# Kernel tuning notes

Measured on AMD Instinct MI355X. Metric: run time of the kernel, lower is better.

## Reference

```python
import jax, jax.numpy as jnp
import numpy as np
import math

B, T, D, H = 16, 256, 1024, 1024
SEG = 16              # segment_len
S = T // SEG          # number of cached segment slots (max_cached_segments=None)
SCALE = 1.0 / math.sqrt(H)


def _ln(x, g, b, eps=1e-5):
    m = jnp.mean(x, -1, keepdims=True)
    v = jnp.mean((x - m) ** 2, -1, keepdims=True)
    return (x - m) * jax.lax.rsqrt(v + eps) * g + b


def _lstm_cell(inp, h, c, Wih, Whh, bih, bhh):
    z = inp @ Wih.T + bih + h @ Whh.T + bhh
    i, f, g, o = jnp.split(z, 4, axis=-1)  # torch LSTMCell gate order i,f,g,o
    c2 = jax.nn.sigmoid(f) * c + jax.nn.sigmoid(i) * jnp.tanh(g)
    return jax.nn.sigmoid(o) * jnp.tanh(c2), c2


def setup_inputs() -> dict:
    key = jax.random.key(0)
    it = iter(jax.random.split(key, 40))

    def un(shape, fan):
        lim = 1.0 / np.sqrt(fan)
        return jax.random.uniform(next(it), shape, jnp.float32, -lim, lim)

    inp = {}
    inp['x'] = jax.random.normal(next(it), (B, T, D), jnp.float32)
    inp['W_ip'] = un((D, D), D); inp['b_ip'] = un((D,), D)
    inp['g_ip'] = jnp.ones((D,), jnp.float32); inp['be_ip'] = jnp.zeros((D,), jnp.float32)
    inp['W_ih0'] = un((4 * H, D), H); inp['W_hh0'] = un((4 * H, H), H)
    inp['b_ih0'] = un((4 * H,), H); inp['b_hh0'] = un((4 * H,), H)
    inp['W_ih1'] = un((4 * H, H), H); inp['W_hh1'] = un((4 * H, H), H)
    inp['b_ih1'] = un((4 * H,), H); inp['b_hh1'] = un((4 * H,), H)
    inp['Wq'] = un((H, H), H); inp['Wk'] = un((H, H), H); inp['Wv'] = un((H, H), H)
    inp['Wg1'] = un((H, 3 * H), 3 * H); inp['bg1'] = un((H,), 3 * H)
    inp['Wg2'] = un((H, H), H); inp['bg2'] = un((H,), H)
    inp['Wo'] = un((H, H), H); inp['bo'] = un((H,), H)
    inp['Wf'] = un((H, 2 * H), 2 * H); inp['bf'] = un((H,), 2 * H)
    inp['g_f'] = jnp.ones((H,), jnp.float32); inp['be_f'] = jnp.zeros((H,), jnp.float32)
    return inp


def reference(x, W_ip, b_ip, g_ip, be_ip,
              W_ih0, W_hh0, b_ih0, b_hh0,
              W_ih1, W_hh1, b_ih1, b_hh1,
              Wq, Wk, Wv, Wg1, bg1, Wg2, bg2, Wo, bo,
              Wf, bf, g_f, be_f):
    # input_proj (eval mode: dropout = identity)
    xp = jax.nn.relu(_ln(x @ W_ip.T + b_ip, g_ip, be_ip))      # [B,T,D]
    xseg = xp.transpose(1, 0, 2).reshape(S, SEG, B, D)          # [S,SEG,B,D]

    def seg_body(carry, xs):
        h0, c0, h1, c1, kbank, vbank = carry
        x_s, s = xs                                             # x_s:[SEG,B,D], s = #cached segments
        valid = jnp.arange(S) < s

        def step(inner, xt):
            h0, c0, h1, c1, seg_sum = inner
            h0, c0 = _lstm_cell(xt, h0, c0, W_ih0, W_hh0, b_ih0, b_hh0)
            h1, c1 = _lstm_cell(h0, h1, c1, W_ih1, W_hh1, b_ih1, b_hh1)
            # SegmentMemoryRetriever, cache_mode='gated_residual'
            q = h1 @ Wq.T
            scores = jnp.einsum('bh,sbh->bs', q, kbank) * SCALE
            scores = jnp.where(valid[None, :], scores, -1e9)
            attn = jax.nn.softmax(scores, axis=-1)
            retrieved = jnp.einsum('bs,sbh->bh', attn, vbank)
            gi = jnp.concatenate([h1, retrieved, h1 - retrieved], -1)
            gate = jax.nn.sigmoid(jax.nn.relu(gi @ Wg1.T + bg1) @ Wg2.T + bg2)
            out = (gate * h1 + (1.0 - gate) * retrieved) @ Wo.T + bo
            ret = jnp.where(s > 0, out, jnp.zeros_like(out))    # empty cache -> zero retrieval
            enh = jax.nn.relu(_ln(jnp.concatenate([h1, ret], -1) @ Wf.T + bf, g_f, be_f))
            return (h0, c0, h1, c1, seg_sum + h1), enh

        init = (h0, c0, h1, c1, jnp.zeros_like(h1))
        (h0, c0, h1, c1, seg_sum), enh = jax.lax.scan(step, init, x_s)
        # append segment to cache; keys/values projected once (linear, equivalent)
        kbank = kbank.at[s].set((seg_sum / SEG) @ Wk.T)         # context = segment mean (use_segment_context)
        vbank = vbank.at[s].set(h1 @ Wv.T)                      # memory = last top hidden of segment
        return (h0, c0, h1, c1, kbank, vbank), enh

    z = jnp.zeros((B, H), x.dtype)
    bank = jnp.zeros((S, B, H), x.dtype)
    carry0 = (z, z, z, z, bank, bank)
    _, enh = jax.lax.scan(seg_body, carry0, (xseg, jnp.arange(S)))
    return enh.reshape(T, B, H).transpose(1, 0, 2)              # sequence_output [B,T,H]
```

## Files before the change

### kernel.cpp

```cpp
#include <hip/hip_runtime.h>
#include <hip/hip_bf16.h>
#include <math.h>

#define B_ 16
#define T_ 256
#define D_ 1024
#define H_ 1024
#define S_ 16
#define SCALE_ (1.0f/32.0f)

typedef __attribute__((ext_vector_type(8))) short short8v;
typedef __attribute__((ext_vector_type(4))) float f32x4;

__device__ __forceinline__ float sigm(float x) { return 1.f / (1.f + expf(-x)); }

__device__ __forceinline__ ushort f2b(float v) {
  __hip_bfloat16 h = __float2bfloat16(v);
  return *reinterpret_cast<ushort*>(&h);
}
__device__ __forceinline__ float b2f(ushort u) {
  union { unsigned u32; float f; } x; x.u32 = ((unsigned)u) << 16; return x.f;
}

__device__ __forceinline__ void glds16(const void* g, void* l) {
  __builtin_amdgcn_global_load_lds((const __attribute__((address_space(1))) void*)g,
                                   (__attribute__((address_space(3))) void*)l, 16, 0, 0);
}

__device__ __forceinline__ void waitflags64(const int* f, int lane) {
  for (;;) {
    int v = __hip_atomic_load(f + lane, __ATOMIC_RELAXED, __HIP_MEMORY_SCOPE_AGENT);
    if (__all(v != 0)) return;
    __builtin_amdgcn_s_sleep(1);
  }
}

__device__ __forceinline__ void publish_pair(ushort* base, int tid, ushort hb) {
  unsigned hi = (unsigned)__shfl_down((int)hb, 1);
  if (!(tid & 1)) {
    unsigned word = (unsigned)hb | (hi << 16);
    __hip_atomic_exchange((unsigned*)base, word,
                          __ATOMIC_RELAXED, __HIP_MEMORY_SCOPE_AGENT);
  }
}

__device__ __forceinline__ float block_sum256(float v) {
  __shared__ float lds[4];
  #pragma unroll
  for (int off = 32; off; off >>= 1) v += __shfl_down(v, off);
  int w = threadIdx.x >> 6;
  if ((threadIdx.x & 63) == 0) lds[w] = v;
  __syncthreads();
  float r = lds[0] + lds[1] + lds[2] + lds[3];
  __syncthreads();
  return r;
}

__global__ __launch_bounds__(256)
void cvt_bf16(const float* __restrict__ in, ushort* __restrict__ out, int n)
{
  int i = (blockIdx.x * 256 + threadIdx.x) * 4;
  if (i >= n) return;
  float4 v = *(const float4*)(in + i);
  ushort4 o; o.x = f2b(v.x); o.y = f2b(v.y); o.z = f2b(v.z); o.w = f2b(v.w);
  *(ushort4*)(out + i) = o;
}

template<int ACT, int REMAP>
__global__ __launch_bounds__(256)
void gemm_bf16(const ushort* __restrict__ A, const ushort* __restrict__ W,
               const float* __restrict__ bias,
               float* __restrict__ Cf, ushort* __restrict__ Cb,
               int M, int N, int K, float ascale)
{
  __shared__ char As[16384];
  __shared__ char Bs[16384];
  const int tid = threadIdx.x;
  const int w = tid >> 6, l = tid & 63;
  const int m0 = blockIdx.y * 128, n0 = blockIdx.x * 128;
  const int wm = w >> 1, wn = w & 1;
  const int srow = l >> 3;
  const int sbyte = ((l & 7) * 16) ^ (srow << 4);
  f32x4 acc[4][4];
  #pragma unroll
  for (int i = 0; i < 4; ++i)
    #pragma unroll
    for (int j = 0; j < 4; ++j) acc[i][j] = (f32x4){0.f, 0.f, 0.f, 0.f};

  for (int k0 = 0; k0 < K; k0 += 64) {
    __syncthreads();
    #pragma unroll
    for (int c = 0; c < 4; ++c) {
      int ca = w * 4 + c;
      int r = ca * 8 + srow;
      glds16((const char*)A + (((size_t)(m0 + r) * K + k0) << 1) + sbyte, As + ca * 1024);
      glds16((const char*)W + (((size_t)(n0 + r) * K + k0) << 1) + sbyte, Bs + ca * 1024);
    }
    __syncthreads();
    #pragma unroll
    for (int ks = 0; ks < 2; ++ks) {
      short8v a[4], b[4];
      int qb = ks * 64 + (l >> 4) * 16;
      #pragma unroll
      for (int i = 0; i < 4; ++i) {
        int ra = wm * 64 + i * 16 + (l & 15);
        a[i] = *(const short8v*)(As + ra * 128 + (qb ^ ((ra & 7) << 4)));
        int rb = wn * 64 + i * 16 + (l & 15);
        b[i] = *(const short8v*)(Bs + rb * 128 + (qb ^ ((rb & 7) << 4)));
      }
      #pragma unroll
      for (int i = 0; i < 4; ++i)
        #pragma unroll
        for (int j = 0; j < 4; ++j)
          acc[i][j] = __builtin_amdgcn_mfma_f32_16x16x32_bf16(a[i], b[j], acc[i][j], 0, 0, 0);
    }
  }
  #pragma unroll
  for (int i = 0; i < 4; ++i) {
    #pragma unroll
    for (int j = 0; j < 4; ++j) {
      int n = n0 + wn * 64 + j * 16 + (l & 15);
      float bv = bias ? bias[n] : 0.f;
      #pragma unroll
      for (int q = 0; q < 4; ++q) {
        int m = m0 + wm * 64 + i * 16 + (l >> 4) * 4 + q;
        float v = acc[i][j][q] * ascale + bv;
        if (ACT == 1) v = fmaxf(v, 0.f);
        if (ACT == 2) v = sigm(v);
        size_t off = REMAP ? ((size_t)((m & 255) * 16 + (m >> 8)) * N + n)
                           : ((size_t)m * N + n);
        if (Cf) Cf[off] = v;
        if (Cb) Cb[off] = f2b(v);
      }
    }
  }
}

__global__ __launch_bounds__(256)
void ln_relu_bf16(const float* __restrict__ X, const float* __restrict__ g,
                  const float* __restrict__ be, ushort* __restrict__ out)
{
  size_t row = blockIdx.x;
  const float4* p = (const float4*)(X + row * 1024);
  int tid = threadIdx.x;
  float4 v = p[tid];
  float s = block_sum256(v.x + v.y + v.z + v.w);
  float mean = s * (1.f / 1024.f);
  float dx = v.x - mean, dy = v.y - mean, dz = v.z - mean, dw = v.w - mean;
  float ss = block_sum256(dx*dx + dy*dy + dz*dz + dw*dw);
  float r = rsqrtf(ss * (1.f / 1024.f) + 1e-5f);
  int c4 = tid * 4;
  ushort4 o;
  o.x = f2b(fmaxf(dx * r * g[c4+0] + be[c4+0], 0.f));
  o.y = f2b(fmaxf(dy * r * g[c4+1] + be[c4+1], 0.f));
  o.z = f2b(fmaxf(dz * r * g[c4+2] + be[c4+2], 0.f));
  o.w = f2b(fmaxf(dw * r * g[c4+3] + be[c4+3], 0.f));
  *(ushort4*)(out + row * 1024 + c4) = o;
}

__global__ __launch_bounds__(256)
void ln_relu_final(const float* __restrict__ F, const float* __restrict__ g,
                   const float* __restrict__ be, float* __restrict__ out)
{
  int row = blockIdx.x;
  int t = row >> 4, b = row & 15;
  const float4* p = (const float4*)(F + (size_t)row * 1024);
  int tid = threadIdx.x;
  float4 v = p[tid];
  float s = block_sum256(v.x + v.y + v.z + v.w);
  float mean = s * (1.f / 1024.f);
  float dx = v.x - mean, dy = v.y - mean, dz = v.z - mean, dw = v.w - mean;
  float ss = block_sum256(dx*dx + dy*dy + dz*dz + dw*dw);
  float r = rsqrtf(ss * (1.f / 1024.f) + 1e-5f);
  int c4 = tid * 4;
  float4 o;
  o.x = fmaxf(dx * r * g[c4+0] + be[c4+0], 0.f);
  o.y = fmaxf(dy * r * g[c4+1] + be[c4+1], 0.f);
  o.z = fmaxf(dz * r * g[c4+2] + be[c4+2], 0.f);
  o.w = fmaxf(dw * r * g[c4+3] + be[c4+3], 0.f);
  ((float4*)(out + ((size_t)b * T_ + t) * 1024))[tid] = o;
}

__global__ __launch_bounds__(512)
void lstm_persistent(const ushort* __restrict__ Z0T,
                     const ushort* __restrict__ whh0,
                     const float* __restrict__ bhh0,
                     const ushort* __restrict__ wih1,
                     const ushort* __restrict__ whh1,
                     const float* __restrict__ bih1,
                     const float* __restrict__ bhh1,
                     ushort* __restrict__ HP,
                     ushort* __restrict__ H1B,
                     const ushort* __restrict__ ZP,
                     float* __restrict__ KSUM,
                     int* flag0,
                     int* flag1)
{
  __shared__ char Ah[65536];
  __shared__ float zs[8][16][16];
  __builtin_amdgcn_fence(__ATOMIC_ACQUIRE, "agent");
  const int tid = threadIdx.x, w = tid >> 6, l = tid & 63;
  const int lm = l & 15, lq = l >> 4;
  const int g = w & 3, kh = w >> 2;
  const int jb = blockIdx.x & 63;
  const int j0 = jb * 16;
  const int eb = tid >> 4, ej = tid & 15, jf = j0 + ej;
  float creg = 0.f;
  float br[4];

  if (blockIdx.x < 64) {
    short8v wreg[16];
    {
      const int n = g * 1024 + j0 + lm;
      const ushort* wb = whh0 + (size_t)n * 1024 + kh * 512 + lq * 8;
      #pragma unroll
      for (int ks = 0; ks < 16; ++ks) wreg[ks] = *(const short8v*)(wb + ks * 32);
    }
    if (tid < 256) {
      #pragma unroll
      for (int gg = 0; gg < 4; ++gg) br[gg] = bhh0[gg * 1024 + jf];
    }
    for (int t = 0; t < T_; ++t) {
      float z0v[4];
      if (tid < 256) {
        const ushort* zp = Z0T + ((size_t)t * 16 + eb) * 4096 + jf;
        #pragma unroll
        for (int gg = 0; gg < 4; ++gg) z0v[gg] = b2f(zp[gg * 1024]);
      }
      if (t > 0) {
        if (w == 0) waitflags64(flag0 + (size_t)t * 64, l);
        __syncthreads();
      }
      const ushort* hin = HP + (size_t)t * 16384;
      #pragma unroll
      for (int it = 0; it < 4; ++it) {
        int g1k = w * 4 + it;
        int kc = g1k * 4 + lq;
        int m = lm ^ (kc & 15);
        glds16(hin + (size_t)m * 1024 + kc * 8, Ah + g1k * 1024);
      }
      __syncthreads();
      {
        f32x4 a0 = {0.f,0.f,0.f,0.f}, a1 = {0.f,0.f,0.f,0.f};
        #pragma unroll
        for (int ks = 0; ks < 16; ks += 2) {
          int kc0 = kh * 64 + ks * 4 + lq;
          int kc1 = kc0 + 4;
          short8v f0 = *(const short8v*)(Ah + kc0 * 256 + ((lm ^ (kc0 & 15)) << 4));
          short8v f1 = *(const short8v*)(Ah + kc1 * 256 + ((lm ^ (kc1 & 15)) << 4));
          a0 = __builtin_amdgcn_mfma_f32_16x16x32_bf16(f0, wreg[ks],     a0, 0, 0, 0);
          a1 = __builtin_amdgcn_mfma_f32_16x16x32_bf16(f1, wreg[ks + 1], a1, 0, 0, 0);
        }
        #pragma unroll
        for (int q = 0; q < 4; ++q) zs[w][lq * 4 + q][lm] = a0[q] + a1[q];
      }
      __syncthreads();
      if (tid < 256) {
        float zi = zs[0][eb][ej] + zs[4][eb][ej] + z0v[0] + br[0];
        float zf = zs[1][eb][ej] + zs[5][eb][ej] + z0v[1] + br[1];
        float zg = zs[2][eb][ej] + zs[6][eb][ej] + z0v[2] + br[2];
        float zo = zs[3][eb][ej] + zs[7][eb][ej] + z0v[3] + br[3];
        float cp = sigm(zf) * creg + sigm(zi) * tanhf(zg);
        creg = cp;
        ushort hb = f2b(sigm(zo) * tanhf(cp));
        publish_pair(HP + (size_t)(t + 1) * 16384 + eb * 1024 + jf, tid, hb);
      }
      __syncthreads();
      if (tid == 0)
        __hip_atomic_store(flag0 + (size_t)(t + 1) * 64 + jb, 1,
                           __ATOMIC_RELAXED, __HIP_MEMORY_SCOPE_AGENT);
    }
  } else {
    short8v wreg[32];
    {
      const int n = g * 1024 + j0 + lm;
      const ushort* wb = (kh ? whh1 : wih1) + (size_t)n * 1024 + lq * 8;
      #pragma unroll
      for (int ks = 0; ks < 32; ++ks) wreg[ks] = *(const short8v*)(wb + ks * 32);
    }
    if (tid < 256) {
      #pragma unroll
      for (int gg = 0; gg < 4; ++gg)
        br[gg] = bih1[gg * 1024 + jf] + bhh1[gg * 1024 + jf];
    }
    float ksr = 0.f;
    for (int t = 0; t < T_; ++t) {
      if (w == 0) waitflags64(flag0 + (size_t)(t + 1) * 64, l);
      __syncthreads();
      const ushort* h0n = HP + (size_t)(t + 1) * 16384;
      #pragma unroll
      for (int it = 0; it < 4; ++it) {
        int g1k = w * 4 + it;
        int kc = g1k * 4 + lq;
        int m = lm ^ (kc & 15);
        glds16(h0n + (size_t)m * 1024 + kc * 8, Ah + g1k * 1024);
      }
      if (w == 1 && t > 0) waitflags64(flag1 + (size_t)(t - 1) * 64, l);
      __syncthreads();
      const ushort* h1p = (t > 0) ? (H1B + (size_t)(t - 1) * 16384) : ZP;
      #pragma unroll
      for (int it = 0; it < 4; ++it) {
        int g1k = 32 + w * 4 + it;
        int kc = g1k * 4 + lq;
        int m = lm ^ (kc & 15);
        glds16(h1p + (size_t)m * 1024 + (kc - 128) * 8, Ah + g1k * 1024);
      }
      __syncthreads();
      {
        f32x4 a0 = {0.f,0.f,0.f,0.f}, a1 = {0.f,0.f,0.f,0.f};
        #pragma unroll
        for (int ks = 0; ks < 32; ks += 2) {
          int kc0 = kh * 128 + ks * 4 + lq;
          int kc1 = kc0 + 4;
          short8v f0 = *(const short8v*)(Ah + kc0 * 256 + ((lm ^ (kc0 & 15)) << 4));
          short8v f1 = *(const short8v*)(Ah + kc1 * 256 + ((lm ^ (kc1 & 15)) << 4));
          a0 = __builtin_amdgcn_mfma_f32_16x16x32_bf16(f0, wreg[ks],     a0, 0, 0, 0);
          a1 = __builtin_amdgcn_mfma_f32_16x16x32_bf16(f1, wreg[ks + 1], a1, 0, 0, 0);
        }
        #pragma unroll
        for (int q = 0; q < 4; ++q) zs[w][lq * 4 + q][lm] = a0[q] + a1[q];
      }
      __syncthreads();
      if (tid < 256) {
        float zi = zs[0][eb][ej] + zs[4][eb][ej] + br[0];
        float zf = zs[1][eb][ej] + zs[5][eb][ej] + br[1];
        float zg = zs[2][eb][ej] + zs[6][eb][ej] + br[2];
        float zo = zs[3][eb][ej] + zs[7][eb][ej] + br[3];
        float cp = sigm(zf) * creg + sigm(zi) * tanhf(zg);
        creg = cp;
        float hv = sigm(zo) * tanhf(cp);
        ksr += hv;
        publish_pair(H1B + (size_t)t * 16384 + eb * 1024 + jf, tid, f2b(hv));
        if ((t & 15) == 15) {
          KSUM[((size_t)(t >> 4) * 16 + eb) * 1024 + jf] = ksr;
          ksr = 0.f;
        }
      }
      __syncthreads();
      if (tid == 0)
        __hip_atomic_store(flag1 + (size_t)t * 64 + jb, 1,
                           __ATOMIC_RELAXED, __HIP_MEMORY_SCOPE_AGENT);
    }
  }
}

__global__ __launch_bounds__(256)
void vgather(const ushort* __restrict__ H1B, ushort* __restrict__ VINB)
{
  int i = blockIdx.x * 256 + threadIdx.x;
  int row = i >> 8, c4 = (i & 255) * 4;
  int src = (row >> 4) * 256 + 240 + (row & 15);
  *(ushort4*)(VINB + (size_t)row * 1024 + c4) =
      *(const ushort4*)(H1B + (size_t)src * 1024 + c4);
}

__global__ __launch_bounds__(256)
void attn_kernel(const float* __restrict__ Q, const float* __restrict__ kbank,
                 const float* __restrict__ vbank, float* __restrict__ R)
{
  int row = blockIdx.x;
  int t = row >> 4, b = row & 15;
  int si = t >> 4;
  int tid = threadIdx.x, lane = tid & 63, w = tid >> 6;
  if (si == 0) {
    float4 z = {0.f, 0.f, 0.f, 0.f};
    ((float4*)(R + (size_t)row * 1024))[tid] = z;
    return;
  }
  __shared__ float sc[16];
  const float* q = Q + (size_t)row * 1024;
  for (int s = w; s < si; s += 4) {
    const float* kk = kbank + ((size_t)s * 16 + b) * 1024;
    float p = 0.f;
    for (int k = lane; k < 1024; k += 64) p += q[k] * kk[k];
    #pragma unroll
    for (int off = 32; off; off >>= 1) p += __shfl_down(p, off);
    if (lane == 0) sc[s] = p * SCALE_;
  }
  __syncthreads();
  float mx = -1e30f;
  for (int s = 0; s < si; ++s) mx = fmaxf(mx, sc[s]);
  float den = 0.f;
  for (int s = 0; s < si; ++s) den += expf(sc[s] - mx);
  float inv = 1.f / den;
  float4 accv = {0.f, 0.f, 0.f, 0.f};
  for (int s = 0; s < si; ++s) {
    float a = expf(sc[s] - mx) * inv;
    float4 vv = ((const float4*)(vbank + ((size_t)s * 16 + b) * 1024))[tid];
    accv.x += a * vv.x; accv.y += a * vv.y; accv.z += a * vv.z; accv.w += a * vv.w;
  }
  ((float4*)(R + (size_t)row * 1024))[tid] = accv;
}

__global__ __launch_bounds__(256)
void build_gi(const ushort* __restrict__ H1B, const float* __restrict__ R,
              ushort* __restrict__ GI)
{
  size_t r = blockIdx.x;
  int c4 = threadIdx.x * 4;
  ushort4 h4 = *(const ushort4*)(H1B + r * 1024 + c4);
  float4 rv = *(const float4*)(R + r * 1024 + c4);
  *(ushort4*)(GI + r * 3072 + c4) = h4;
  ushort4 rb; rb.x = f2b(rv.x); rb.y = f2b(rv.y); rb.z = f2b(rv.z); rb.w = f2b(rv.w);
  *(ushort4*)(GI + r * 3072 + 1024 + c4) = rb;
  ushort4 d;
  d.x = f2b(b2f(h4.x) - rv.x); d.y = f2b(b2f(h4.y) - rv.y);
  d.z = f2b(b2f(h4.z) - rv.z); d.w = f2b(b2f(h4.w) - rv.w);
  *(ushort4*)(GI + r * 3072 + 2048 + c4) = d;
}

__global__ __launch_bounds__(256)
void build_mix(const float* __restrict__ G, const ushort* __restrict__ H1B,
               const float* __restrict__ R, ushort* __restrict__ M)
{
  size_t r = blockIdx.x;
  int c4 = threadIdx.x * 4;
  float4 g = *(const float4*)(G + r * 1024 + c4);
  ushort4 h = *(const ushort4*)(H1B + r * 1024 + c4);
  float4 rv = *(const float4*)(R + r * 1024 + c4);
  ushort4 o;
  o.x = f2b(g.x * b2f(h.x) + (1.f - g.x) * rv.x);
  o.y = f2b(g.y * b2f(h.y) + (1.f - g.y) * rv.y);
  o.z = f2b(g.z * b2f(h.z) + (1.f - g.z) * rv.z);
  o.w = f2b(g.w * b2f(h.w) + (1.f - g.w) * rv.w);
  *(ushort4*)(M + r * 1024 + c4) = o;
}

__global__ __launch_bounds__(256)
void build_cat(const ushort* __restrict__ H1B, const float* __restrict__ O,
               ushort* __restrict__ C)
{
  size_t r = blockIdx.x;
  int c4 = threadIdx.x * 4;
  *(ushort4*)(C + r * 2048 + c4) = *(const ushort4*)(H1B + r * 1024 + c4);
  ushort4 o;
  if (r >= 256) {
    float4 v = *(const float4*)(O + r * 1024 + c4);
    o.x = f2b(v.x); o.y = f2b(v.y); o.z = f2b(v.z); o.w = f2b(v.w);
  } else { o.x = o.y = o.z = o.w = 0; }
  *(ushort4*)(C + r * 2048 + 1024 + c4) = o;
}

extern "C" void kernel_launch(void* const* d_in, const int* in_sizes, int n_in,
                              void* d_out, int out_size, void* d_ws, size_t ws_size,
                              hipStream_t stream) {
  const float* x     = (const float*)d_in[0];
  const float* W_ip  = (const float*)d_in[1];
  const float* b_ip  = (const float*)d_in[2];
  const float* g_ip  = (const float*)d_in[3];
  const float* be_ip = (const float*)d_in[4];
  const float* W_ih0 = (const float*)d_in[5];
  const float* W_hh0 = (const float*)d_in[6];
  const float* b_ih0 = (const float*)d_in[7];
  const float* b_hh0 = (const float*)d_in[8];
  const float* W_ih1 = (const float*)d_in[9];
  const float* W_hh1 = (const float*)d_in[10];
  const float* b_ih1 = (const float*)d_in[11];
  const float* b_hh1 = (const float*)d_in[12];
  const float* Wq    = (const float*)d_in[13];
  const float* Wk    = (const float*)d_in[14];
  const float* Wv    = (const float*)d_in[15];
  const float* Wg1   = (const float*)d_in[16];
  const float* bg1   = (const float*)d_in[17];
  const float* Wg2   = (const float*)d_in[18];
  const float* bg2   = (const float*)d_in[19];
  const float* Wo    = (const float*)d_in[20];
  const float* bo    = (const float*)d_in[21];
  const float* Wf    = (const float*)d_in[22];
  const float* bff   = (const float*)d_in[23];
  const float* g_f   = (const float*)d_in[24];
  const float* be_f  = (const float*)d_in[25];
  float* out = (float*)d_out;
  char* ws = (char*)d_ws;
  const size_t MB = (size_t)1 << 20;
  const size_t KB = (size_t)1 << 10;

  ushort* WB = (ushort*)(ws);
  ushort* wipB  = WB;
  ushort* wih0B = WB + 1*1048576;
  ushort* whh0B = WB + 5*1048576;
  ushort* wih1B = WB + 9*1048576;
  ushort* whh1B = WB + 13*1048576;
  ushort* wqB   = WB + 17*1048576;
  ushort* wkB   = WB + 18*1048576;
  ushort* wvB   = WB + 19*1048576;
  ushort* wg1B  = WB + 20*1048576;
  ushort* wg2B  = WB + 23*1048576;
  ushort* woB   = WB + 24*1048576;
  ushort* wfB   = WB + 25*1048576;

  ushort* XB   = (ushort*)(ws + 54 * MB);
  float*  XP   = (float*)(ws + 62 * MB);
  float*  Qf   = XP;
  char*   SCR  = ws + 78 * MB;
  ushort* Z0T  = (ushort*)SCR;
  ushort* GIB  = (ushort*)SCR;
  ushort* G1B  = (ushort*)(SCR + 24 * MB);
  float*  GT   = (float*)(SCR + 32 * MB);
  ushort* MIXB = (ushort*)SCR;
  float*  OUTB = (float*)(SCR + 8 * MB);
  ushort* CATB = (ushort*)(SCR + 24 * MB);
  float*  FB   = (float*)SCR;
  ushort* H1B  = (ushort*)(ws + 126 * MB);
  ushort* HP   = (ushort*)(ws + 134 * MB);
  float*  R    = (float*)(ws + 134 * MB);
  char*   ST   = ws + 150 * MB;
  int*    flag0 = (int*)(ST);
  int*    flag1 = (int*)(ST + 68 * KB);
  const ushort* ZPc = (const ushort*)(ST + 132 * KB);
  float*  KSUM = (float*)(ST + 192 * KB);
  ushort* KSB  = (ushort*)(ST + 1216 * KB);
  float*  KBf  = (float*)(ST + 1728 * KB);
  float*  VBf  = (float*)(ST + 2752 * KB);
  ushort* VINB = (ushort*)(ST + 3776 * KB);

  hipMemsetAsync(ST, 0, 164 * KB, stream);
  hipMemsetAsync(HP, 0, 32 * KB, stream);

  dim3 blk(256);
  auto cvt = [&](const float* src, ushort* dst, int n) {
    cvt_bf16<<<dim3((n / 4 + 255) / 256), blk, 0, stream>>>(src, dst, n);
  };
  cvt(x,     XB,    4194304);
  cvt(W_ip,  wipB,  1048576);
  cvt(W_ih0, wih0B, 4194304);
  cvt(W_hh0, whh0B, 4194304);
  cvt(W_ih1, wih1B, 4194304);
  cvt(W_hh1, whh1B, 4194304);
  cvt(Wq,    wqB,   1048576);
  cvt(Wk,    wkB,   1048576);
  cvt(Wv,    wvB,   1048576);
  cvt(Wg1,   wg1B,  3145728);
  cvt(Wg2,   wg2B,  1048576);
  cvt(Wo,    woB,   1048576);
  cvt(Wf,    wfB,   2097152);

  gemm_bf16<0,0><<<dim3(1024/128, 4096/128), blk, 0, stream>>>(
      XB, wipB, b_ip, XP, nullptr, 4096, 1024, 1024, 1.f);
  ln_relu_bf16<<<4096, blk, 0, stream>>>(XP, g_ip, be_ip, XB);
  gemm_bf16<0,1><<<dim3(4096/128, 4096/128), blk, 0, stream>>>(
      XB, wih0B, b_ih0, nullptr, Z0T, 4096, 4096, 1024, 1.f);
  {
    void* kargs[] = {
      (void*)&Z0T, (void*)&whh0B, (void*)&b_hh0,
      (void*)&wih1B, (void*)&whh1B, (void*)&b_ih1, (void*)&b_hh1,
      (void*)&HP, (void*)&H1B, (void*)&ZPc, (void*)&KSUM,
      (void*)&flag0, (void*)&flag1
    };
    hipLaunchCooperativeKernel((const void*)lstm_persistent,
                               dim3(128), dim3(512), kargs, 0, stream);
  }
  cvt(KSUM, KSB, 262144);
  gemm_bf16<0,0><<<dim3(1024/128, 256/128), blk, 0, stream>>>(
      KSB, wkB, nullptr, KBf, nullptr, 256, 1024, 1024, 1.f/16.f);
  vgather<<<256, blk, 0, stream>>>(H1B, VINB);
  gemm_bf16<0,0><<<dim3(1024/128, 256/128), blk, 0, stream>>>(
      VINB, wvB, nullptr, VBf, nullptr, 256, 1024, 1024, 1.f);
  gemm_bf16<0,0><<<dim3(1024/128, 4096/128), blk, 0, stream>>>(
      H1B, wqB, nullptr, Qf, nullptr, 4096, 1024, 1024, 1.f);
  attn_kernel<<<4096, blk, 0, stream>>>(Qf, KBf, VBf, R);
  build_gi<<<4096, blk, 0, stream>>>(H1B, R, GIB);
  gemm_bf16<1,0><<<dim3(1024/128, 4096/128), blk, 0, stream>>>(
      GIB, wg1B, bg1, nullptr, G1B, 4096, 1024, 3072, 1.f);
  gemm_bf16<2,0><<<dim3(1024/128, 4096/128), blk, 0, stream>>>(
      G1B, wg2B, bg2, GT, nullptr, 4096, 1024, 1024, 1.f);
  build_mix<<<4096, blk, 0, stream>>>(GT, H1B, R, MIXB);
  gemm_bf16<0,0><<<dim3(1024/128, 4096/128), blk, 0, stream>>>(
      MIXB, woB, bo, OUTB, nullptr, 4096, 1024, 1024, 1.f);
  build_cat<<<4096, blk, 0, stream>>>(H1B, OUTB, CATB);
  gemm_bf16<0,0><<<dim3(1024/128, 4096/128), blk, 0, stream>>>(
      CATB, wfB, bff, FB, nullptr, 4096, 1024, 2048, 1.f);
  ln_relu_final<<<4096, blk, 0, stream>>>(FB, g_f, be_f, out);
}
```

Measured before the change: 1.464 ms.

## Fuse elementwise gate-mix and concat into GEMM epilogues; batch weight conversions

```diff
diff --git a/kernel.cpp b/kernel.cpp
--- a/kernel.cpp
+++ b/kernel.cpp
@@ -56,6 +56,27 @@
   return r;
 }
 
+#define NJOBS 14
+struct CvtJobs {
+  const float* src[NJOBS];
+  ushort* dst[NJOBS];
+  int cum[NJOBS + 1];
+};
+
+__global__ __launch_bounds__(256)
+void cvt_all(CvtJobs J)
+{
+  int i = blockIdx.x * 256 + threadIdx.x;
+  if (i >= J.cum[NJOBS]) return;
+  int j = 0;
+  #pragma unroll
+  for (int k = 1; k < NJOBS; ++k) j += (i >= J.cum[k]) ? 1 : 0;
+  int idx = i - J.cum[j];
+  float4 v = ((const float4*)J.src[j])[idx];
+  ushort4 o; o.x = f2b(v.x); o.y = f2b(v.y); o.z = f2b(v.z); o.w = f2b(v.w);
+  ((ushort4*)J.dst[j])[idx] = o;
+}
+
 __global__ __launch_bounds__(256)
 void cvt_bf16(const float* __restrict__ in, ushort* __restrict__ out, int n)
 {
@@ -71,7 +92,8 @@
 void gemm_bf16(const ushort* __restrict__ A, const ushort* __restrict__ W,
                const float* __restrict__ bias,
                float* __restrict__ Cf, ushort* __restrict__ Cb,
-               int M, int N, int K, float ascale)
+               int M, int N, int K, float ascale, int ldc,
+               const ushort* __restrict__ Hx, const float* __restrict__ Rx)
 {
   __shared__ char As[16384];
   __shared__ char Bs[16384];
@@ -127,8 +149,15 @@
         float v = acc[i][j][q] * ascale + bv;
         if (ACT == 1) v = fmaxf(v, 0.f);
         if (ACT == 2) v = sigm(v);
-        size_t off = REMAP ? ((size_t)((m & 255) * 16 + (m >> 8)) * N + n)
-                           : ((size_t)m * N + n);
+        if (ACT == 3) {
+          float gte = sigm(v);
+          float h = b2f(Hx[(size_t)m * 1024 + n]);
+          float r = Rx[(size_t)m * 1024 + n];
+          v = gte * h + (1.f - gte) * r;
+        }
+        if (ACT == 4) v = (m >= 256) ? v : 0.f;
+        size_t off = REMAP ? ((size_t)((m & 255) * 16 + (m >> 8)) * ldc + n)
+                           : ((size_t)m * ldc + n);
         if (Cf) Cf[off] = v;
         if (Cb) Cb[off] = f2b(v);
       }
@@ -393,8 +422,8 @@
 }
 
 __global__ __launch_bounds__(256)
-void build_gi(const ushort* __restrict__ H1B, const float* __restrict__ R,
-              ushort* __restrict__ GI)
+void build_gi_cat(const ushort* __restrict__ H1B, const float* __restrict__ R,
+                  ushort* __restrict__ GI, ushort* __restrict__ CATB)
 {
   size_t r = blockIdx.x;
   int c4 = threadIdx.x * 4;
@@ -407,38 +436,7 @@
   d.x = f2b(b2f(h4.x) - rv.x); d.y = f2b(b2f(h4.y) - rv.y);
   d.z = f2b(b2f(h4.z) - rv.z); d.w = f2b(b2f(h4.w) - rv.w);
   *(ushort4*)(GI + r * 3072 + 2048 + c4) = d;
-}
-
-__global__ __launch_bounds__(256)
-void build_mix(const float* __restrict__ G, const ushort* __restrict__ H1B,
-               const float* __restrict__ R, ushort* __restrict__ M)
-{
-  size_t r = blockIdx.x;
-  int c4 = threadIdx.x * 4;
-  float4 g = *(const float4*)(G + r * 1024 + c4);
-  ushort4 h = *(const ushort4*)(H1B + r * 1024 + c4);
-  float4 rv = *(const float4*)(R + r * 1024 + c4);
-  ushort4 o;
-  o.x = f2b(g.x * b2f(h.x) + (1.f - g.x) * rv.x);
-  o.y = f2b(g.y * b2f(h.y) + (1.f - g.y) * rv.y);
-  o.z = f2b(g.z * b2f(h.z) + (1.f - g.z) * rv.z);
-  o.w = f2b(g.w * b2f(h.w) + (1.f - g.w) * rv.w);
-  *(ushort4*)(M + r * 1024 + c4) = o;
-}
-
-__global__ __launch_bounds__(256)
-void build_cat(const ushort* __restrict__ H1B, const float* __restrict__ O,
-               ushort* __restrict__ C)
-{
-  size_t r = blockIdx.x;
-  int c4 = threadIdx.x * 4;
-  *(ushort4*)(C + r * 2048 + c4) = *(const ushort4*)(H1B + r * 1024 + c4);
-  ushort4 o;
-  if (r >= 256) {
-    float4 v = *(const float4*)(O + r * 1024 + c4);
-    o.x = f2b(v.x); o.y = f2b(v.y); o.z = f2b(v.z); o.w = f2b(v.w);
-  } else { o.x = o.y = o.z = o.w = 0; }
-  *(ushort4*)(C + r * 2048 + 1024 + c4) = o;
+  *(ushort4*)(CATB + r * 2048 + c4) = h4;
 }
 
 extern "C" void kernel_launch(void* const* d_in, const int* in_sizes, int n_in,
@@ -495,11 +493,9 @@
   char*   SCR  = ws + 78 * MB;
   ushort* Z0T  = (ushort*)SCR;
   ushort* GIB  = (ushort*)SCR;
-  ushort* G1B  = (ushort*)(SCR + 24 * MB);
-  float*  GT   = (float*)(SCR + 32 * MB);
+  ushort* CATB = (ushort*)(SCR + 24 * MB);
+  ushort* G1B  = (ushort*)(SCR + 40 * MB);
   ushort* MIXB = (ushort*)SCR;
-  float*  OUTB = (float*)(SCR + 8 * MB);
-  ushort* CATB = (ushort*)(SCR + 24 * MB);
   float*  FB   = (float*)SCR;
   ushort* H1B  = (ushort*)(ws + 126 * MB);
   ushort* HP   = (ushort*)(ws + 134 * MB);
@@ -518,28 +514,31 @@
   hipMemsetAsync(HP, 0, 32 * KB, stream);
 
   dim3 blk(256);
-  auto cvt = [&](const float* src, ushort* dst, int n) {
-    cvt_bf16<<<dim3((n / 4 + 255) / 256), blk, 0, stream>>>(src, dst, n);
-  };
-  cvt(x,     XB,    4194304);
-  cvt(W_ip,  wipB,  1048576);
-  cvt(W_ih0, wih0B, 4194304);
-  cvt(W_hh0, whh0B, 4194304);
-  cvt(W_ih1, wih1B, 4194304);
-  cvt(W_hh1, whh1B, 4194304);
-  cvt(Wq,    wqB,   1048576);
-  cvt(Wk,    wkB,   1048576);
-  cvt(Wv,    wvB,   1048576);
-  cvt(Wg1,   wg1B,  3145728);
-  cvt(Wg2,   wg2B,  1048576);
-  cvt(Wo,    woB,   1048576);
-  cvt(Wf,    wfB,   2097152);
+  {
+    CvtJobs J;
+    const float* srcs[NJOBS] = { x, W_ip, W_ih0, W_hh0, W_ih1, W_hh1,
+                                 Wq, Wk, Wv, Wg1, Wg2, Wo, Wf, nullptr };
+    ushort* dsts[NJOBS] = { XB, wipB, wih0B, whh0B, wih1B, whh1B,
+                            wqB, wkB, wvB, wg1B, wg2B, woB, wfB, nullptr };
+    int n4[NJOBS] = { 1048576, 262144, 1048576, 1048576, 1048576, 1048576,
+                      262144, 262144, 262144, 786432, 262144, 262144,
+                      524288, 0 };
+    int c = 0;
+    for (int j = 0; j < NJOBS; ++j) {
+      J.src[j] = srcs[j] ? srcs[j] : x;
+      J.dst[j] = dsts[j] ? dsts[j] : XB;
+      J.cum[j] = c;
+      c += n4[j];
+    }
+    J.cum[NJOBS] = c;
+    cvt_all<<<dim3((c + 255) / 256), blk, 0, stream>>>(J);
+  }
 
   gemm_bf16<0,0><<<dim3(1024/128, 4096/128), blk, 0, stream>>>(
-      XB, wipB, b_ip, XP, nullptr, 4096, 1024, 1024, 1.f);
+      XB, wipB, b_ip, XP, nullptr, 4096, 1024, 1024, 1.f, 1024, nullptr, nullptr);
   ln_relu_bf16<<<4096, blk, 0, stream>>>(XP, g_ip, be_ip, XB);
   gemm_bf16<0,1><<<dim3(4096/128, 4096/128), blk, 0, stream>>>(
-      XB, wih0B, b_ih0, nullptr, Z0T, 4096, 4096, 1024, 1.f);
+      XB, wih0B, b_ih0, nullptr, Z0T, 4096, 4096, 1024, 1.f, 4096, nullptr, nullptr);
   {
     void* kargs[] = {
       (void*)&Z0T, (void*)&whh0B, (void*)&b_hh0,
@@ -550,25 +549,23 @@
     hipLaunchCooperativeKernel((const void*)lstm_persistent,
                                dim3(128), dim3(512), kargs, 0, stream);
   }
-  cvt(KSUM, KSB, 262144);
+  cvt_bf16<<<dim3(262144/4/256), blk, 0, stream>>>(KSUM, KSB, 262144);
   gemm_bf16<0,0><<<dim3(1024/128, 256/128), blk, 0, stream>>>(
-      KSB, wkB, nullptr, KBf, nullptr, 256, 1024, 1024, 1.f/16.f);
+      KSB, wkB, nullptr, KBf, nullptr, 256, 1024, 1024, 1.f/16.f, 1024, nullptr, nullptr);
   vgather<<<256, blk, 0, stream>>>(H1B, VINB);
   gemm_bf16<0,0><<<dim3(1024/128, 256/128), blk, 0, stream>>>(
-      VINB, wvB, nullptr, VBf, nullptr, 256, 1024, 1024, 1.f);
+      VINB, wvB, nullptr, VBf, nullptr, 256, 1024, 1024, 1.f, 1024, nullptr, nullptr);
   gemm_bf16<0,0><<<dim3(1024/128, 4096/128), blk, 0, stream>>>(
-      H1B, wqB, nullptr, Qf, nullptr, 4096, 1024, 1024, 1.f);
+      H1B, wqB, nullptr, Qf, nullptr, 4096, 1024, 1024, 1.f, 1024, nullptr, nullptr);
   attn_kernel<<<4096, blk, 0, stream>>>(Qf, KBf, VBf, R);
-  build_gi<<<4096, blk, 0, stream>>>(H1B, R, GIB);
+  build_gi_cat<<<4096, blk, 0, stream>>>(H1B, R, GIB, CATB);
   gemm_bf16<1,0><<<dim3(1024/128, 4096/128), blk, 0, stream>>>(
-      GIB, wg1B, bg1, nullptr, G1B, 4096, 1024, 3072, 1.f);
-  gemm_bf16<2,0><<<dim3(1024/128, 4096/128), blk, 0, stream>>>(
-      G1B, wg2B, bg2, GT, nullptr, 4096, 1024, 1024, 1.f);
-  build_mix<<<4096, blk, 0, stream>>>(GT, H1B, R, MIXB);
+      GIB, wg1B, bg1, nullptr, G1B, 4096, 1024, 3072, 1.f, 1024, nullptr, nullptr);
+  gemm_bf16<3,0><<<dim3(1024/128, 4096/128), blk, 0, stream>>>(
+      G1B, wg2B, bg2, nullptr, MIXB, 4096, 1024, 1024, 1.f, 1024, H1B, R);
+  gemm_bf16<4,0><<<dim3(1024/128, 4096/128), blk, 0, stream>>>(
+      MIXB, woB, bo, nullptr, CATB + 1024, 4096, 1024, 1024, 1.f, 2048, nullptr, nullptr);
   gemm_bf16<0,0><<<dim3(1024/128, 4096/128), blk, 0, stream>>>(
-      MIXB, woB, bo, OUTB, nullptr, 4096, 1024, 1024, 1.f);
-  build_cat<<<4096, blk, 0, stream>>>(H1B, OUTB, CATB);
-  gemm_bf16<0,0><<<dim3(1024/128, 4096/128), blk, 0, stream>>>(
-      CATB, wfB, bff, FB, nullptr, 4096, 1024, 2048, 1.f);
+      CATB, wfB, bff, FB, nullptr, 4096, 1024, 2048, 1.f, 1024, nullptr, nullptr);
   ln_relu_final<<<4096, blk, 0, stream>>>(FB, g_f, be_f, out);
 }
```

New measurement: 1.413 ms. 1.04x faster.
